# Kernel optimization log

Measured on AMD Instinct MI355X. Metric: run time of the kernel, lower is better.

Reference implementation:

```python
import jax, jax.numpy as jnp
import numpy as np

T, H, E, I = 1024, 1024, 64, 512          # tokens, hidden, n_routed_experts, moe_intermediate
NG, TKG, TOPK = 8, 3, 6                   # n_group, topk_group, num_experts_per_tok
NSH = 2                                   # n_shared_experts
RSF = 2.5                                 # routed_scaling_factor
SI = NSH * I                              # shared-expert intermediate


def setup_inputs() -> dict:
    key = jax.random.key(0)
    ks = jax.random.split(key, 9)
    s = 0.02
    return {
        "hidden_states": jax.random.normal(ks[0], (T, H), jnp.float32),
        "gate_w": jax.random.normal(ks[1], (H, E), jnp.float32) * s,
        "e_bias": jax.random.normal(ks[2], (E,), jnp.float32) * s,
        "w_gate": jax.random.normal(ks[3], (E, H, I), jnp.float32) * s,
        "w_up": jax.random.normal(ks[4], (E, H, I), jnp.float32) * s,
        "w_down": jax.random.normal(ks[5], (E, I, H), jnp.float32) * s,
        "sw_gate": jax.random.normal(ks[6], (H, SI), jnp.float32) * s,
        "sw_up": jax.random.normal(ks[7], (H, SI), jnp.float32) * s,
        "sw_down": jax.random.normal(ks[8], (SI, H), jnp.float32) * s,
    }


def _silu_mlp(x, wg, wu, wd):
    # DeepseekV2MLP: down( silu(gate(x)) * up(x) )
    return (jax.nn.silu(x @ wg) * (x @ wu)) @ wd


def _grouped_topk(logits, e_bias):
    # noaux_tc: sigmoid scoring; bias only influences selection, not weights
    scores = jax.nn.sigmoid(logits)                       # [T, E]
    sc = scores + e_bias
    # group score = sum of top-2 biased scores within each group
    gsc = jax.lax.top_k(sc.reshape(-1, NG, E // NG), 2)[0].sum(-1)   # [T, NG]
    gidx = jax.lax.top_k(gsc, TKG)[1]                     # [T, TKG]
    rows = jnp.arange(sc.shape[0])[:, None]
    gmask = jnp.zeros_like(gsc).at[rows, gidx].set(1.0)   # [T, NG]
    emask = jnp.repeat(gmask, E // NG, axis=1) > 0        # [T, E]
    masked = jnp.where(emask, sc, -jnp.inf)
    topk_ids = jax.lax.top_k(masked, TOPK)[1]             # [T, TOPK]
    w = jnp.take_along_axis(scores, topk_ids, axis=1)     # unbiased scores
    w = w / w.sum(-1, keepdims=True)                      # renormalize (norm_topk_prob)
    return w, topk_ids


def reference(hidden_states, gate_w, e_bias, w_gate, w_up, w_down, sw_gate, sw_up, sw_down):
    x = hidden_states
    logits = x @ gate_w                                   # [T, E]
    w, ids = _grouped_topk(logits, e_bias)
    rows = jnp.arange(x.shape[0])[:, None]
    dense_w = jnp.zeros((x.shape[0], E), x.dtype).at[rows, ids].set(w)  # [T, E]

    def body(acc, ws):
        wg, wu, wd, we = ws                               # we: [T] combine weights for this expert
        return acc + we[:, None] * _silu_mlp(x, wg, wu, wd), None

    routed, _ = jax.lax.scan(body, jnp.zeros_like(x), (w_gate, w_up, w_down, dense_w.T))
    shared = _silu_mlp(x, sw_gate, sw_up, sw_down)
    return routed * RSF + shared
```

## Files before the change

kernel.cpp:

```cpp
#include <hip/hip_runtime.h>
#include <hip/hip_bf16.h>

#define T_TOK 1024
#define HDIM  1024
#define NEXP  64
#define IDIM  512
#define SIDIM 1024
#define NGRP  8
#define GSZ   8
#define TKGN  3
#define TOPKN 6
#define CAPS  14336

typedef __attribute__((ext_vector_type(8))) short bf16x8;
typedef __attribute__((ext_vector_type(4))) float f32x4;

__device__ __forceinline__ short f2bf(float f) {
  union { __hip_bfloat16 h; short s; } u;
  u.h = __float2bfloat16(f);
  return u.s;
}

__global__ void k0_init(int* counts, int* cursor, float4* out4) {
  int gid = blockIdx.x * blockDim.x + threadIdx.x;
  if (gid < NEXP) { counts[gid] = 0; cursor[gid] = 0; }
  int total4 = T_TOK * HDIM / 4;
  int stride = gridDim.x * blockDim.x;
  for (int i = gid; i < total4; i += stride)
    out4[i] = make_float4(0.f, 0.f, 0.f, 0.f);
}

__global__ __launch_bounds__(256) void k1_gate(
    const float* __restrict__ x, const float* __restrict__ gw,
    const float* __restrict__ ebias,
    int* __restrict__ ids, float* __restrict__ wts, int* __restrict__ counts) {
  int sub = threadIdx.x >> 6;
  int lane = threadIdx.x & 63;
  int t = blockIdx.x * 4 + sub;
  const float* xr = x + (size_t)t * HDIM;
  double a0 = 0.0, a1 = 0.0, a2 = 0.0, a3 = 0.0;
  for (int h = 0; h < HDIM; h += 4) {
    float4 xv = *(const float4*)(xr + h);
    a0 += (double)xv.x * (double)gw[(h + 0) * NEXP + lane];
    a1 += (double)xv.y * (double)gw[(h + 1) * NEXP + lane];
    a2 += (double)xv.z * (double)gw[(h + 2) * NEXP + lane];
    a3 += (double)xv.w * (double)gw[(h + 3) * NEXP + lane];
  }
  float logit = (float)((a0 + a1) + (a2 + a3));
  float sig = 1.f / (1.f + expf(-logit));
  float sc = sig + ebias[lane];
  __shared__ float s_sc[4][NEXP], s_sig[4][NEXP];
  s_sc[sub][lane] = sc; s_sig[sub][lane] = sig;
  __syncthreads();
  if (lane == 0) {
    const float* ssc = s_sc[sub];
    const float* ssig = s_sig[sub];
    float gsum[NGRP];
    for (int g = 0; g < NGRP; ++g) {
      float m1 = -1e30f; int i1 = -1;
      for (int i = 0; i < GSZ; ++i) {
        float v = ssc[g * GSZ + i];
        if (v > m1) { m1 = v; i1 = i; }
      }
      float m2 = -1e30f;
      for (int i = 0; i < GSZ; ++i) {
        if (i == i1) continue;
        float v = ssc[g * GSZ + i];
        if (v > m2) m2 = v;
      }
      gsum[g] = m1 + m2;
    }
    unsigned gselmask = 0;
    for (int r = 0; r < TKGN; ++r) {
      float best = -1e30f; int bi = 0;
      for (int g = 0; g < NGRP; ++g) {
        if ((gselmask >> g) & 1) continue;
        if (gsum[g] > best) { best = gsum[g]; bi = g; }
      }
      gselmask |= 1u << bi;
    }
    unsigned long long taken = 0;
    int chosen[TOPKN]; float wsum = 0.f;
    for (int r = 0; r < TOPKN; ++r) {
      float best = -1e30f; int bi = 0;
      for (int e = 0; e < NEXP; ++e) {
        if (!((gselmask >> (e >> 3)) & 1)) continue;
        if ((taken >> e) & 1) continue;
        float v = ssc[e];
        if (v > best) { best = v; bi = e; }
      }
      taken |= 1ull << bi;
      chosen[r] = bi;
      wsum += ssig[bi];
    }
    for (int r = 0; r < TOPKN; ++r) {
      ids[t * TOPKN + r] = chosen[r];
      wts[t * TOPKN + r] = ssig[chosen[r]] / wsum;
      atomicAdd(&counts[chosen[r]], 1);
    }
  }
}

__global__ void k1b_scan(const int* __restrict__ counts, int* __restrict__ eoff,
                         int* __restrict__ tile_e, int* __restrict__ tile_base,
                         int* __restrict__ nt_p,
                         int* __restrict__ slot_tok, float* __restrict__ slot_wt) {
  __shared__ int soff[NEXP + 1];
  __shared__ int s_total;
  int tid = threadIdx.x;
  if (tid == 0) {
    int o = 0, idx = 0;
    for (int e = 0; e < NEXP; ++e) {
      soff[e] = o;
      int ntile = (counts[e] + 127) >> 7;
      for (int t2 = 0; t2 < ntile; ++t2) { tile_e[idx] = e; tile_base[idx] = o + t2 * 128; ++idx; }
      o += ntile << 7;
    }
    soff[NEXP] = o; nt_p[0] = idx; s_total = o;
  }
  __syncthreads();
  if (tid <= NEXP) eoff[tid] = soff[tid];
  int total = s_total;
  for (int i = tid; i < total; i += blockDim.x) { slot_tok[i] = 0; slot_wt[i] = 0.f; }
}

__global__ void k1c_fill(const int* __restrict__ ids, const float* __restrict__ wts,
                         const int* __restrict__ eoff, int* __restrict__ cursor,
                         int* __restrict__ slot_tok, float* __restrict__ slot_wt) {
  int i = blockIdx.x * blockDim.x + threadIdx.x;
  if (i >= T_TOK * TOPKN) return;
  int e = ids[i];
  int s = eoff[e] + atomicAdd(&cursor[e], 1);
  slot_tok[s] = i / TOPKN;
  slot_wt[s] = wts[i] * 2.5f;
}

__device__ __forceinline__ void tile_mid(
    const float* __restrict__ x, const float* __restrict__ wg, const float* __restrict__ wu,
    const int* __restrict__ slot_tok, int rowbase, int ic0, int IC,
    __hip_bfloat16* __restrict__ mid,
    short* As, short* Bg, short* Bu) {
  int tid = threadIdx.x;
  int wave = tid >> 6, lane = tid & 63;
  int wm = wave >> 1, wn = wave & 1;
  int lr = lane & 15, lk = lane >> 4;

  int ar = tid >> 3, ac8 = (tid & 7) << 3;
  const float* aptr[2];
  #pragma unroll
  for (int it = 0; it < 2; ++it) {
    int r = ar + it * 64;
    int tok = slot_tok ? slot_tok[rowbase + r] : (rowbase + r);
    aptr[it] = x + (size_t)tok * HDIM + ac8;
  }
  int bn = tid & 63, bkg = tid >> 6;
  const float* bgp = wg + (size_t)(bkg * 8) * IC + ic0 + bn;
  const float* bup = wu + (size_t)(bkg * 8) * IC + ic0 + bn;
  int bgran = (bn * 8 + (bkg ^ (bn & 7))) * 8;

  f32x4 accg[2][2], accu[2][2];
  #pragma unroll
  for (int a = 0; a < 2; ++a)
    #pragma unroll
    for (int b = 0; b < 2; ++b) { accg[a][b] = (f32x4)0.f; accu[a][b] = (f32x4)0.f; }

  float bgr[8], bur[8];
  #pragma unroll
  for (int i = 0; i < 8; ++i) {
    bgr[i] = bgp[(size_t)i * IC];
    bur[i] = bup[(size_t)i * IC];
  }

  const int NST = HDIM / 64;
  for (int s = 0; s < NST; ++s) {
    int k0 = s * 64;
    float4 av[2][2];
    #pragma unroll
    for (int it = 0; it < 2; ++it) {
      av[it][0] = *(const float4*)(aptr[it] + k0);
      av[it][1] = *(const float4*)(aptr[it] + k0 + 4);
    }
    __syncthreads();
    #pragma unroll
    for (int it = 0; it < 2; ++it) {
      bf16x8 tv;
      tv[0] = f2bf(av[it][0].x); tv[1] = f2bf(av[it][0].y);
      tv[2] = f2bf(av[it][0].z); tv[3] = f2bf(av[it][0].w);
      tv[4] = f2bf(av[it][1].x); tv[5] = f2bf(av[it][1].y);
      tv[6] = f2bf(av[it][1].z); tv[7] = f2bf(av[it][1].w);
      *(bf16x8*)&As[(ar + it * 64) * 72 + ac8] = tv;
    }
    {
      bf16x8 tg, tu;
      #pragma unroll
      for (int i = 0; i < 8; ++i) { tg[i] = f2bf(bgr[i]); tu[i] = f2bf(bur[i]); }
      *(bf16x8*)&Bg[bgran] = tg;
      *(bf16x8*)&Bu[bgran] = tu;
    }
    __syncthreads();
    if (s + 1 < NST) {
      #pragma unroll
      for (int i = 0; i < 8; ++i) {
        bgr[i] = bgp[(size_t)(k0 + 64 + i) * IC];
        bur[i] = bup[(size_t)(k0 + 64 + i) * IC];
      }
    }
    #pragma unroll
    for (int kk = 0; kk < 2; ++kk) {
      bf16x8 af[2];
      #pragma unroll
      for (int mf = 0; mf < 2; ++mf) {
        int row = wm * 32 + mf * 16 + lr;
        af[mf] = *(bf16x8*)&As[row * 72 + kk * 32 + lk * 8];
      }
      #pragma unroll
      for (int nf = 0; nf < 2; ++nf) {
        int col = wn * 32 + nf * 16 + lr;
        int gidx = (col * 8 + ((kk * 4 + lk) ^ (col & 7))) * 8;
        bf16x8 bgf = *(bf16x8*)&Bg[gidx];
        bf16x8 buf_ = *(bf16x8*)&Bu[gidx];
        #pragma unroll
        for (int mf = 0; mf < 2; ++mf) {
          accg[mf][nf] = __builtin_amdgcn_mfma_f32_16x16x32_bf16(af[mf], bgf, accg[mf][nf], 0, 0, 0);
          accu[mf][nf] = __builtin_amdgcn_mfma_f32_16x16x32_bf16(af[mf], buf_, accu[mf][nf], 0, 0, 0);
        }
      }
    }
  }
  #pragma unroll
  for (int mf = 0; mf < 2; ++mf)
    #pragma unroll
    for (int nf = 0; nf < 2; ++nf)
      #pragma unroll
      for (int r = 0; r < 4; ++r) {
        int row = wm * 32 + mf * 16 + lk * 4 + r;
        int col = wn * 32 + nf * 16 + lr;
        float gv = accg[mf][nf][r], uv = accu[mf][nf][r];
        float h = gv / (1.f + expf(-gv)) * uv;
        mid[(size_t)(rowbase + row) * IC + ic0 + col] = __float2bfloat16(h);
      }
}

__device__ __forceinline__ void tile_down(
    const __hip_bfloat16* __restrict__ mid, const float* __restrict__ wd,
    const int* __restrict__ slot_tok, const float* __restrict__ slot_wt,
    int rowbase, int n0, int KD,
    float* __restrict__ out, short* As, short* Bs) {
  int tid = threadIdx.x;
  int wave = tid >> 6, lane = tid & 63;
  int wm = wave >> 1, wn = wave & 1;
  int lr = lane & 15, lk = lane >> 4;

  int ar = tid >> 3, ac8 = (tid & 7) << 3;
  const __hip_bfloat16* aptr[2];
  #pragma unroll
  for (int it = 0; it < 2; ++it)
    aptr[it] = mid + (size_t)(rowbase + ar + it * 64) * KD + ac8;

  int bn = tid & 63, bkg = tid >> 6;
  const float* bp = wd + (size_t)(bkg * 8) * HDIM + n0 + bn;
  int bgran = (bn * 8 + (bkg ^ (bn & 7))) * 8;

  f32x4 acc[2][2];
  #pragma unroll
  for (int a = 0; a < 2; ++a)
    #pragma unroll
    for (int b = 0; b < 2; ++b) acc[a][b] = (f32x4)0.f;

  float br[8];
  #pragma unroll
  for (int i = 0; i < 8; ++i) br[i] = bp[(size_t)i * HDIM];

  const int NST_ = KD / 64;
  for (int s = 0; s < NST_; ++s) {
    int k0 = s * 64;
    bf16x8 avv[2];
    #pragma unroll
    for (int it = 0; it < 2; ++it)
      avv[it] = *(const bf16x8*)(aptr[it] + k0);
    __syncthreads();
    #pragma unroll
    for (int it = 0; it < 2; ++it)
      *(bf16x8*)&As[(ar + it * 64) * 72 + ac8] = avv[it];
    {
      bf16x8 tb;
      #pragma unroll
      for (int i = 0; i < 8; ++i) tb[i] = f2bf(br[i]);
      *(bf16x8*)&Bs[bgran] = tb;
    }
    __syncthreads();
    if (s + 1 < NST_) {
      #pragma unroll
      for (int i = 0; i < 8; ++i)
        br[i] = bp[(size_t)(k0 + 64 + i) * HDIM];
    }
    #pragma unroll
    for (int kk = 0; kk < 2; ++kk) {
      bf16x8 af[2];
      #pragma unroll
      for (int mf = 0; mf < 2; ++mf) {
        int row = wm * 32 + mf * 16 + lr;
        af[mf] = *(bf16x8*)&As[row * 72 + kk * 32 + lk * 8];
      }
      #pragma unroll
      for (int nf = 0; nf < 2; ++nf) {
        int col = wn * 32 + nf * 16 + lr;
        bf16x8 bf_ = *(bf16x8*)&Bs[(col * 8 + ((kk * 4 + lk) ^ (col & 7))) * 8];
        #pragma unroll
        for (int mf = 0; mf < 2; ++mf)
          acc[mf][nf] = __builtin_amdgcn_mfma_f32_16x16x32_bf16(af[mf], bf_, acc[mf][nf], 0, 0, 0);
      }
    }
  }
  #pragma unroll
  for (int mf = 0; mf < 2; ++mf)
    #pragma unroll
    for (int nf = 0; nf < 2; ++nf)
      #pragma unroll
      for (int r = 0; r < 4; ++r) {
        int row = wm * 32 + mf * 16 + lk * 4 + r;
        int col = wn * 32 + nf * 16 + lr;
        float v = acc[mf][nf][r];
        if (slot_wt) {
          int s = rowbase + row;
          float w = slot_wt[s];
          if (w != 0.f) {
            int tok = slot_tok[s];
            atomicAdd(&out[(size_t)tok * HDIM + n0 + col], v * w);
          }
        } else {
          atomicAdd(&out[(size_t)(rowbase + row) * HDIM + n0 + col], v);
        }
      }
}

__global__ __launch_bounds__(512) void k2_fused(
    const float* __restrict__ x, const float* __restrict__ Wg, const float* __restrict__ Wu,
    const float* __restrict__ swg, const float* __restrict__ swu,
    const int* __restrict__ slot_tok, const int* __restrict__ tile_e,
    const int* __restrict__ tile_base, const int* __restrict__ nt_p,
    __hip_bfloat16* __restrict__ mid_r, __hip_bfloat16* __restrict__ mid_s) {
  __shared__ __align__(16) short As[128 * 72];
  __shared__ __align__(16) short Bg[64 * 64];
  __shared__ __align__(16) short Bu[64 * 64];
  int nrt = nt_p[0] * 8;
  int nitems = nrt + 128;
  for (int item = blockIdx.x; item < nitems; item += gridDim.x) {
    if (item < nrt) {
      int tile = item >> 3, c = item & 7;
      int e = tile_e[tile];
      tile_mid(x, Wg + (size_t)e * HDIM * IDIM, Wu + (size_t)e * HDIM * IDIM,
               slot_tok, tile_base[tile], c * 64, IDIM, mid_r, As, Bg, Bu);
    } else {
      int it = item - nrt;
      int mt = it >> 4, c = it & 15;
      tile_mid(x, swg, swu, nullptr, mt * 128, c * 64, SIDIM, mid_s, As, Bg, Bu);
    }
  }
}

__global__ __launch_bounds__(512) void k3_fused(
    const __hip_bfloat16* __restrict__ mid_r, const __hip_bfloat16* __restrict__ mid_s,
    const float* __restrict__ Wd, const float* __restrict__ swd,
    const int* __restrict__ slot_tok, const float* __restrict__ slot_wt,
    const int* __restrict__ tile_e, const int* __restrict__ tile_base,
    const int* __restrict__ nt_p, float* __restrict__ out) {
  __shared__ __align__(16) short As[128 * 72];
  __shared__ __align__(16) short Bs[64 * 64];
  int nrt = nt_p[0] * 16;
  int nsh = 128;
  int nitems = nrt + nsh;
  for (int item = blockIdx.x; item < nitems; item += gridDim.x) {
    if (item < nsh) {
      int mt = item >> 4, c = item & 15;
      tile_down(mid_s, swd, nullptr, nullptr, mt * 128, c * 64, SIDIM, out, As, Bs);
    } else {
      int it = item - nsh;
      int tile = it >> 4, c = it & 15;
      int e = tile_e[tile];
      tile_down(mid_r, Wd + (size_t)e * IDIM * HDIM, slot_tok, slot_wt,
                tile_base[tile], c * 64, IDIM, out, As, Bs);
    }
  }
}

extern "C" void kernel_launch(void* const* d_in, const int* in_sizes, int n_in,
                              void* d_out, int out_size, void* d_ws, size_t ws_size,
                              hipStream_t stream) {
  (void)in_sizes; (void)n_in; (void)out_size; (void)ws_size;
  const float* x      = (const float*)d_in[0];
  const float* gate_w = (const float*)d_in[1];
  const float* ebias  = (const float*)d_in[2];
  const float* wgate  = (const float*)d_in[3];
  const float* wup    = (const float*)d_in[4];
  const float* wdown  = (const float*)d_in[5];
  const float* swg    = (const float*)d_in[6];
  const float* swu    = (const float*)d_in[7];
  const float* swd    = (const float*)d_in[8];
  float* out = (float*)d_out;

  char* ws = (char*)d_ws;
  int*   counts    = (int*)(ws + 0);
  int*   cursor    = (int*)(ws + 256);
  int*   eoff      = (int*)(ws + 512);
  int*   nt_p      = (int*)(ws + 1024);
  int*   tile_e    = (int*)(ws + 1088);
  int*   tile_base = (int*)(ws + 1600);
  int*   ids       = (int*)(ws + 4096);
  float* wts       = (float*)(ws + 28672);
  int*   slot_tok  = (int*)(ws + 53248);
  float* slot_wt   = (float*)(ws + 110592);
  __hip_bfloat16* mid_r = (__hip_bfloat16*)(ws + 167936);
  __hip_bfloat16* mid_s = mid_r + (size_t)CAPS * IDIM;

  k0_init<<<256, 256, 0, stream>>>(counts, cursor, (float4*)out);
  k1_gate<<<T_TOK / 4, 256, 0, stream>>>(x, gate_w, ebias, ids, wts, counts);
  k1b_scan<<<1, 256, 0, stream>>>(counts, eoff, tile_e, tile_base, nt_p, slot_tok, slot_wt);
  k1c_fill<<<(T_TOK * TOPKN + 255) / 256, 256, 0, stream>>>(ids, wts, eoff, cursor, slot_tok, slot_wt);
  k2_fused<<<640, 512, 0, stream>>>(x, wgate, wup, swg, swu, slot_tok, tile_e, tile_base, nt_p, mid_r, mid_s);
  k3_fused<<<1152, 512, 0, stream>>>(mid_r, mid_s, wdown, swd, slot_tok, slot_wt, tile_e, tile_base, nt_p, out);
}
```

Before: 263.3 us.

## Double-buffer GEMM LDS tiles and replace atomic scatter with bf16 outputs plus combine

Both GEMM tile routines now use double-buffered, XOR-swizzled LDS for A and B. Global loads for stage s+2 are issued while stage s computes, and only one barrier runs per stage. The down-projection no longer scatters fp32 atomicAdds into the output. It writes per-slot bf16 results, and a new k4_combine kernel gathers each token's six expert rows plus the shared row, weighted by the routing weights. This removes atomic contention and the output zeroing pass, at the cost of extra bf16 intermediate traffic, bf16 rounding of partial outputs, and one more launch.

```diff
diff --git a/kernel.cpp b/kernel.cpp
--- a/kernel.cpp
+++ b/kernel.cpp
@@ -20,14 +20,17 @@
   u.h = __float2bfloat16(f);
   return u.s;
 }
-
-__global__ void k0_init(int* counts, int* cursor, float4* out4) {
-  int gid = blockIdx.x * blockDim.x + threadIdx.x;
-  if (gid < NEXP) { counts[gid] = 0; cursor[gid] = 0; }
-  int total4 = T_TOK * HDIM / 4;
-  int stride = gridDim.x * blockDim.x;
-  for (int i = gid; i < total4; i += stride)
-    out4[i] = make_float4(0.f, 0.f, 0.f, 0.f);
+__device__ __forceinline__ float bf2f(short s) {
+  union { float f; unsigned u; } c;
+  c.u = ((unsigned)(unsigned short)s) << 16;
+  return c.f;
+}
+
+#define BARRIER() asm volatile("s_waitcnt lgkmcnt(0)\n\ts_barrier" ::: "memory")
+
+__global__ void k0_init(int* counts, int* cursor) {
+  int i = threadIdx.x;
+  if (i < NEXP) { counts[i] = 0; cursor[i] = 0; }
 }
 
 __global__ __launch_bounds__(256) void k1_gate(
@@ -103,8 +106,7 @@
 
 __global__ void k1b_scan(const int* __restrict__ counts, int* __restrict__ eoff,
                          int* __restrict__ tile_e, int* __restrict__ tile_base,
-                         int* __restrict__ nt_p,
-                         int* __restrict__ slot_tok, float* __restrict__ slot_wt) {
+                         int* __restrict__ nt_p, int* __restrict__ slot_tok) {
   __shared__ int soff[NEXP + 1];
   __shared__ int s_total;
   int tid = threadIdx.x;
@@ -121,42 +123,41 @@
   __syncthreads();
   if (tid <= NEXP) eoff[tid] = soff[tid];
   int total = s_total;
-  for (int i = tid; i < total; i += blockDim.x) { slot_tok[i] = 0; slot_wt[i] = 0.f; }
-}
-
-__global__ void k1c_fill(const int* __restrict__ ids, const float* __restrict__ wts,
+  for (int i = tid; i < total; i += blockDim.x) slot_tok[i] = 0;
+}
+
+__global__ void k1c_fill(const int* __restrict__ ids,
                          const int* __restrict__ eoff, int* __restrict__ cursor,
-                         int* __restrict__ slot_tok, float* __restrict__ slot_wt) {
+                         int* __restrict__ slot_tok, int* __restrict__ tslot) {
   int i = blockIdx.x * blockDim.x + threadIdx.x;
   if (i >= T_TOK * TOPKN) return;
   int e = ids[i];
   int s = eoff[e] + atomicAdd(&cursor[e], 1);
   slot_tok[s] = i / TOPKN;
-  slot_wt[s] = wts[i] * 2.5f;
+  tslot[i] = s;
 }
 
 __device__ __forceinline__ void tile_mid(
     const float* __restrict__ x, const float* __restrict__ wg, const float* __restrict__ wu,
     const int* __restrict__ slot_tok, int rowbase, int ic0, int IC,
-    __hip_bfloat16* __restrict__ mid,
-    short* As, short* Bg, short* Bu) {
+    __hip_bfloat16* __restrict__ mid, short* As, short* Bg, short* Bu) {
   int tid = threadIdx.x;
   int wave = tid >> 6, lane = tid & 63;
   int wm = wave >> 1, wn = wave & 1;
   int lr = lane & 15, lk = lane >> 4;
 
-  int ar = tid >> 3, ac8 = (tid & 7) << 3;
-  const float* aptr[2];
-  #pragma unroll
-  for (int it = 0; it < 2; ++it) {
-    int r = ar + it * 64;
-    int tok = slot_tok ? slot_tok[rowbase + r] : (rowbase + r);
-    aptr[it] = x + (size_t)tok * HDIM + ac8;
-  }
+  int ar = tid >> 3, kg = tid & 7;
+  int aw0 = (ar * 8 + (kg ^ (ar & 7))) * 8;
+  int aw1 = ((ar + 64) * 8 + (kg ^ (ar & 7))) * 8;
+  int tok0 = slot_tok ? slot_tok[rowbase + ar] : (rowbase + ar);
+  int tok1 = slot_tok ? slot_tok[rowbase + ar + 64] : (rowbase + ar + 64);
+  const float* aptr0 = x + (size_t)tok0 * HDIM + kg * 8;
+  const float* aptr1 = x + (size_t)tok1 * HDIM + kg * 8;
+
   int bn = tid & 63, bkg = tid >> 6;
   const float* bgp = wg + (size_t)(bkg * 8) * IC + ic0 + bn;
   const float* bup = wu + (size_t)(bkg * 8) * IC + ic0 + bn;
-  int bgran = (bn * 8 + (bkg ^ (bn & 7))) * 8;
+  int bw = (bn * 8 + (bkg ^ (bn & 7))) * 8;
 
   f32x4 accg[2][2], accu[2][2];
   #pragma unroll
@@ -164,61 +165,55 @@
     #pragma unroll
     for (int b = 0; b < 2; ++b) { accg[a][b] = (f32x4)0.f; accu[a][b] = (f32x4)0.f; }
 
+  float4 a00, a01, a10, a11;
   float bgr[8], bur[8];
-  #pragma unroll
-  for (int i = 0; i < 8; ++i) {
-    bgr[i] = bgp[(size_t)i * IC];
-    bur[i] = bup[(size_t)i * IC];
-  }
-
-  const int NST = HDIM / 64;
-  for (int s = 0; s < NST; ++s) {
-    int k0 = s * 64;
-    float4 av[2][2];
-    #pragma unroll
-    for (int it = 0; it < 2; ++it) {
-      av[it][0] = *(const float4*)(aptr[it] + k0);
-      av[it][1] = *(const float4*)(aptr[it] + k0 + 4);
-    }
-    __syncthreads();
-    #pragma unroll
-    for (int it = 0; it < 2; ++it) {
-      bf16x8 tv;
-      tv[0] = f2bf(av[it][0].x); tv[1] = f2bf(av[it][0].y);
-      tv[2] = f2bf(av[it][0].z); tv[3] = f2bf(av[it][0].w);
-      tv[4] = f2bf(av[it][1].x); tv[5] = f2bf(av[it][1].y);
-      tv[6] = f2bf(av[it][1].z); tv[7] = f2bf(av[it][1].w);
-      *(bf16x8*)&As[(ar + it * 64) * 72 + ac8] = tv;
-    }
-    {
-      bf16x8 tg, tu;
-      #pragma unroll
-      for (int i = 0; i < 8; ++i) { tg[i] = f2bf(bgr[i]); tu[i] = f2bf(bur[i]); }
-      *(bf16x8*)&Bg[bgran] = tg;
-      *(bf16x8*)&Bu[bgran] = tu;
-    }
-    __syncthreads();
-    if (s + 1 < NST) {
-      #pragma unroll
-      for (int i = 0; i < 8; ++i) {
-        bgr[i] = bgp[(size_t)(k0 + 64 + i) * IC];
-        bur[i] = bup[(size_t)(k0 + 64 + i) * IC];
-      }
-    }
+
+  auto LOAD = [&](int s) {
+    const float* p0 = aptr0 + s * 64;
+    const float* p1 = aptr1 + s * 64;
+    a00 = *(const float4*)p0; a01 = *(const float4*)(p0 + 4);
+    a10 = *(const float4*)p1; a11 = *(const float4*)(p1 + 4);
+    #pragma unroll
+    for (int i = 0; i < 8; ++i) {
+      bgr[i] = bgp[(size_t)(s * 64 + i) * IC];
+      bur[i] = bup[(size_t)(s * 64 + i) * IC];
+    }
+  };
+  auto STORE = [&](int b) {
+    short* as = As + b * 8192;
+    short* bg = Bg + b * 4096;
+    short* bu = Bu + b * 4096;
+    bf16x8 t0, t1;
+    t0[0] = f2bf(a00.x); t0[1] = f2bf(a00.y); t0[2] = f2bf(a00.z); t0[3] = f2bf(a00.w);
+    t0[4] = f2bf(a01.x); t0[5] = f2bf(a01.y); t0[6] = f2bf(a01.z); t0[7] = f2bf(a01.w);
+    t1[0] = f2bf(a10.x); t1[1] = f2bf(a10.y); t1[2] = f2bf(a10.z); t1[3] = f2bf(a10.w);
+    t1[4] = f2bf(a11.x); t1[5] = f2bf(a11.y); t1[6] = f2bf(a11.z); t1[7] = f2bf(a11.w);
+    *(bf16x8*)&as[aw0] = t0;
+    *(bf16x8*)&as[aw1] = t1;
+    bf16x8 tg, tu;
+    #pragma unroll
+    for (int i = 0; i < 8; ++i) { tg[i] = f2bf(bgr[i]); tu[i] = f2bf(bur[i]); }
+    *(bf16x8*)&bg[bw] = tg;
+    *(bf16x8*)&bu[bw] = tu;
+  };
+  auto COMPUTE = [&](int b) {
+    const short* as = As + b * 8192;
+    const short* bg = Bg + b * 4096;
+    const short* bu = Bu + b * 4096;
     #pragma unroll
     for (int kk = 0; kk < 2; ++kk) {
       bf16x8 af[2];
       #pragma unroll
       for (int mf = 0; mf < 2; ++mf) {
         int row = wm * 32 + mf * 16 + lr;
-        af[mf] = *(bf16x8*)&As[row * 72 + kk * 32 + lk * 8];
+        af[mf] = *(const bf16x8*)&as[(row * 8 + ((kk * 4 + lk) ^ (row & 7))) * 8];
       }
       #pragma unroll
       for (int nf = 0; nf < 2; ++nf) {
         int col = wn * 32 + nf * 16 + lr;
-        int gidx = (col * 8 + ((kk * 4 + lk) ^ (col & 7))) * 8;
-        bf16x8 bgf = *(bf16x8*)&Bg[gidx];
-        bf16x8 buf_ = *(bf16x8*)&Bu[gidx];
+        int gi = (col * 8 + ((kk * 4 + lk) ^ (col & 7))) * 8;
+        bf16x8 bgf = *(const bf16x8*)&bg[gi];
+        bf16x8 buf_ = *(const bf16x8*)&bu[gi];
         #pragma unroll
         for (int mf = 0; mf < 2; ++mf) {
           accg[mf][nf] = __builtin_amdgcn_mfma_f32_16x16x32_bf16(af[mf], bgf, accg[mf][nf], 0, 0, 0);
@@ -226,7 +221,22 @@
         }
       }
     }
-  }
+  };
+
+  const int NST = HDIM / 64;
+  LOAD(0);
+  STORE(0);
+  LOAD(1);
+  BARRIER();
+  for (int s = 0; s < NST; ++s) {
+    COMPUTE(s & 1);
+    if (s + 1 < NST) {
+      STORE((s + 1) & 1);
+      if (s + 2 < NST) LOAD(s + 2);
+      BARRIER();
+    }
+  }
+
   #pragma unroll
   for (int mf = 0; mf < 2; ++mf)
     #pragma unroll
@@ -243,23 +253,22 @@
 
 __device__ __forceinline__ void tile_down(
     const __hip_bfloat16* __restrict__ mid, const float* __restrict__ wd,
-    const int* __restrict__ slot_tok, const float* __restrict__ slot_wt,
     int rowbase, int n0, int KD,
-    float* __restrict__ out, short* As, short* Bs) {
+    __hip_bfloat16* __restrict__ dout, short* As, short* Bs) {
   int tid = threadIdx.x;
   int wave = tid >> 6, lane = tid & 63;
   int wm = wave >> 1, wn = wave & 1;
   int lr = lane & 15, lk = lane >> 4;
 
-  int ar = tid >> 3, ac8 = (tid & 7) << 3;
-  const __hip_bfloat16* aptr[2];
-  #pragma unroll
-  for (int it = 0; it < 2; ++it)
-    aptr[it] = mid + (size_t)(rowbase + ar + it * 64) * KD + ac8;
+  int ar = tid >> 3, kg = tid & 7;
+  int aw0 = (ar * 8 + (kg ^ (ar & 7))) * 8;
+  int aw1 = ((ar + 64) * 8 + (kg ^ (ar & 7))) * 8;
+  const __hip_bfloat16* aptr0 = mid + (size_t)(rowbase + ar) * KD + kg * 8;
+  const __hip_bfloat16* aptr1 = mid + (size_t)(rowbase + ar + 64) * KD + kg * 8;
 
   int bn = tid & 63, bkg = tid >> 6;
   const float* bp = wd + (size_t)(bkg * 8) * HDIM + n0 + bn;
-  int bgran = (bn * 8 + (bkg ^ (bn & 7))) * 8;
+  int bw = (bn * 8 + (bkg ^ (bn & 7))) * 8;
 
   f32x4 acc[2][2];
   #pragma unroll
@@ -267,51 +276,61 @@
     #pragma unroll
     for (int b = 0; b < 2; ++b) acc[a][b] = (f32x4)0.f;
 
+  bf16x8 av0, av1;
   float br[8];
-  #pragma unroll
-  for (int i = 0; i < 8; ++i) br[i] = bp[(size_t)i * HDIM];
-
-  const int NST_ = KD / 64;
-  for (int s = 0; s < NST_; ++s) {
-    int k0 = s * 64;
-    bf16x8 avv[2];
-    #pragma unroll
-    for (int it = 0; it < 2; ++it)
-      avv[it] = *(const bf16x8*)(aptr[it] + k0);
-    __syncthreads();
-    #pragma unroll
-    for (int it = 0; it < 2; ++it)
-      *(bf16x8*)&As[(ar + it * 64) * 72 + ac8] = avv[it];
-    {
-      bf16x8 tb;
-      #pragma unroll
-      for (int i = 0; i < 8; ++i) tb[i] = f2bf(br[i]);
-      *(bf16x8*)&Bs[bgran] = tb;
-    }
-    __syncthreads();
-    if (s + 1 < NST_) {
-      #pragma unroll
-      for (int i = 0; i < 8; ++i)
-        br[i] = bp[(size_t)(k0 + 64 + i) * HDIM];
-    }
+
+  auto LOAD = [&](int s) {
+    av0 = *(const bf16x8*)(aptr0 + s * 64);
+    av1 = *(const bf16x8*)(aptr1 + s * 64);
+    #pragma unroll
+    for (int i = 0; i < 8; ++i) br[i] = bp[(size_t)(s * 64 + i) * HDIM];
+  };
+  auto STORE = [&](int b) {
+    short* as = As + b * 8192;
+    short* bs = Bs + b * 4096;
+    *(bf16x8*)&as[aw0] = av0;
+    *(bf16x8*)&as[aw1] = av1;
+    bf16x8 tb;
+    #pragma unroll
+    for (int i = 0; i < 8; ++i) tb[i] = f2bf(br[i]);
+    *(bf16x8*)&bs[bw] = tb;
+  };
+  auto COMPUTE = [&](int b) {
+    const short* as = As + b * 8192;
+    const short* bs = Bs + b * 4096;
     #pragma unroll
     for (int kk = 0; kk < 2; ++kk) {
       bf16x8 af[2];
       #pragma unroll
       for (int mf = 0; mf < 2; ++mf) {
         int row = wm * 32 + mf * 16 + lr;
-        af[mf] = *(bf16x8*)&As[row * 72 + kk * 32 + lk * 8];
+        af[mf] = *(const bf16x8*)&as[(row * 8 + ((kk * 4 + lk) ^ (row & 7))) * 8];
       }
       #pragma unroll
       for (int nf = 0; nf < 2; ++nf) {
         int col = wn * 32 + nf * 16 + lr;
-        bf16x8 bf_ = *(bf16x8*)&Bs[(col * 8 + ((kk * 4 + lk) ^ (col & 7))) * 8];
+        bf16x8 bf_ = *(const bf16x8*)&bs[(col * 8 + ((kk * 4 + lk) ^ (col & 7))) * 8];
         #pragma unroll
         for (int mf = 0; mf < 2; ++mf)
           acc[mf][nf] = __builtin_amdgcn_mfma_f32_16x16x32_bf16(af[mf], bf_, acc[mf][nf], 0, 0, 0);
       }
     }
-  }
+  };
+
+  const int NST = KD / 64;
+  LOAD(0);
+  STORE(0);
+  LOAD(1);
+  BARRIER();
+  for (int s = 0; s < NST; ++s) {
+    COMPUTE(s & 1);
+    if (s + 1 < NST) {
+      STORE((s + 1) & 1);
+      if (s + 2 < NST) LOAD(s + 2);
+      BARRIER();
+    }
+  }
+
   #pragma unroll
   for (int mf = 0; mf < 2; ++mf)
     #pragma unroll
@@ -320,17 +339,7 @@
       for (int r = 0; r < 4; ++r) {
         int row = wm * 32 + mf * 16 + lk * 4 + r;
         int col = wn * 32 + nf * 16 + lr;
-        float v = acc[mf][nf][r];
-        if (slot_wt) {
-          int s = rowbase + row;
-          float w = slot_wt[s];
-          if (w != 0.f) {
-            int tok = slot_tok[s];
-            atomicAdd(&out[(size_t)tok * HDIM + n0 + col], v * w);
-          }
-        } else {
-          atomicAdd(&out[(size_t)(rowbase + row) * HDIM + n0 + col], v);
-        }
+        dout[(size_t)(rowbase + row) * HDIM + n0 + col] = __float2bfloat16(acc[mf][nf][r]);
       }
 }
 
@@ -340,9 +349,9 @@
     const int* __restrict__ slot_tok, const int* __restrict__ tile_e,
     const int* __restrict__ tile_base, const int* __restrict__ nt_p,
     __hip_bfloat16* __restrict__ mid_r, __hip_bfloat16* __restrict__ mid_s) {
-  __shared__ __align__(16) short As[128 * 72];
-  __shared__ __align__(16) short Bg[64 * 64];
-  __shared__ __align__(16) short Bu[64 * 64];
+  __shared__ __align__(16) short As[2 * 8192];
+  __shared__ __align__(16) short Bg[2 * 4096];
+  __shared__ __align__(16) short Bu[2 * 4096];
   int nrt = nt_p[0] * 8;
   int nitems = nrt + 128;
   for (int item = blockIdx.x; item < nitems; item += gridDim.x) {
@@ -362,26 +371,56 @@
 __global__ __launch_bounds__(512) void k3_fused(
     const __hip_bfloat16* __restrict__ mid_r, const __hip_bfloat16* __restrict__ mid_s,
     const float* __restrict__ Wd, const float* __restrict__ swd,
-    const int* __restrict__ slot_tok, const float* __restrict__ slot_wt,
     const int* __restrict__ tile_e, const int* __restrict__ tile_base,
-    const int* __restrict__ nt_p, float* __restrict__ out) {
-  __shared__ __align__(16) short As[128 * 72];
-  __shared__ __align__(16) short Bs[64 * 64];
+    const int* __restrict__ nt_p,
+    __hip_bfloat16* __restrict__ dout_r, __hip_bfloat16* __restrict__ dout_s) {
+  __shared__ __align__(16) short As[2 * 8192];
+  __shared__ __align__(16) short Bs[2 * 4096];
   int nrt = nt_p[0] * 16;
   int nsh = 128;
   int nitems = nrt + nsh;
   for (int item = blockIdx.x; item < nitems; item += gridDim.x) {
     if (item < nsh) {
       int mt = item >> 4, c = item & 15;
-      tile_down(mid_s, swd, nullptr, nullptr, mt * 128, c * 64, SIDIM, out, As, Bs);
+      tile_down(mid_s, swd, mt * 128, c * 64, SIDIM, dout_s, As, Bs);
     } else {
       int it = item - nsh;
       int tile = it >> 4, c = it & 15;
       int e = tile_e[tile];
-      tile_down(mid_r, Wd + (size_t)e * IDIM * HDIM, slot_tok, slot_wt,
-                tile_base[tile], c * 64, IDIM, out, As, Bs);
-    }
-  }
+      tile_down(mid_r, Wd + (size_t)e * IDIM * HDIM, tile_base[tile], c * 64, IDIM,
+                dout_r, As, Bs);
+    }
+  }
+}
+
+__global__ __launch_bounds__(128) void k4_combine(
+    const __hip_bfloat16* __restrict__ dout_r, const __hip_bfloat16* __restrict__ dout_s,
+    const int* __restrict__ tslot, const float* __restrict__ wts,
+    float* __restrict__ out) {
+  int t = blockIdx.x;
+  int tid = threadIdx.x;
+  int sl[TOPKN]; float w[TOPKN];
+  #pragma unroll
+  for (int r = 0; r < TOPKN; ++r) {
+    sl[r] = tslot[t * TOPKN + r];
+    w[r] = wts[t * TOPKN + r] * 2.5f;
+  }
+  int h0 = tid * 8;
+  float acc[8];
+  bf16x8 vs = *(const bf16x8*)((const short*)dout_s + (size_t)t * HDIM + h0);
+  #pragma unroll
+  for (int j = 0; j < 8; ++j) acc[j] = bf2f(vs[j]);
+  #pragma unroll
+  for (int r = 0; r < TOPKN; ++r) {
+    bf16x8 v = *(const bf16x8*)((const short*)dout_r + (size_t)sl[r] * HDIM + h0);
+    #pragma unroll
+    for (int j = 0; j < 8; ++j) acc[j] += w[r] * bf2f(v[j]);
+  }
+  float* op = out + (size_t)t * HDIM + h0;
+  float4 o0 = make_float4(acc[0], acc[1], acc[2], acc[3]);
+  float4 o1 = make_float4(acc[4], acc[5], acc[6], acc[7]);
+  *(float4*)op = o0;
+  *(float4*)(op + 4) = o1;
 }
 
 extern "C" void kernel_launch(void* const* d_in, const int* in_sizes, int n_in,
@@ -408,15 +447,18 @@
   int*   tile_base = (int*)(ws + 1600);
   int*   ids       = (int*)(ws + 4096);
   float* wts       = (float*)(ws + 28672);
-  int*   slot_tok  = (int*)(ws + 53248);
-  float* slot_wt   = (float*)(ws + 110592);
-  __hip_bfloat16* mid_r = (__hip_bfloat16*)(ws + 167936);
-  __hip_bfloat16* mid_s = mid_r + (size_t)CAPS * IDIM;
-
-  k0_init<<<256, 256, 0, stream>>>(counts, cursor, (float4*)out);
+  int*   tslot     = (int*)(ws + 53248);
+  int*   slot_tok  = (int*)(ws + 77824);
+  __hip_bfloat16* mid_r  = (__hip_bfloat16*)(ws + 135168);
+  __hip_bfloat16* mid_s  = mid_r + (size_t)CAPS * IDIM;
+  __hip_bfloat16* dout_r = (__hip_bfloat16*)(ws + 16912384);
+  __hip_bfloat16* dout_s = dout_r + (size_t)CAPS * HDIM;
+
+  k0_init<<<1, 128, 0, stream>>>(counts, cursor);
   k1_gate<<<T_TOK / 4, 256, 0, stream>>>(x, gate_w, ebias, ids, wts, counts);
-  k1b_scan<<<1, 256, 0, stream>>>(counts, eoff, tile_e, tile_base, nt_p, slot_tok, slot_wt);
-  k1c_fill<<<(T_TOK * TOPKN + 255) / 256, 256, 0, stream>>>(ids, wts, eoff, cursor, slot_tok, slot_wt);
+  k1b_scan<<<1, 256, 0, stream>>>(counts, eoff, tile_e, tile_base, nt_p, slot_tok);
+  k1c_fill<<<(T_TOK * TOPKN + 255) / 256, 256, 0, stream>>>(ids, eoff, cursor, slot_tok, tslot);
   k2_fused<<<640, 512, 0, stream>>>(x, wgate, wup, swg, swu, slot_tok, tile_e, tile_base, nt_p, mid_r, mid_s);
-  k3_fused<<<1152, 512, 0, stream>>>(mid_r, mid_s, wdown, swd, slot_tok, slot_wt, tile_e, tile_base, nt_p, out);
-}
+  k3_fused<<<1152, 512, 0, stream>>>(mid_r, mid_s, wdown, swd, tile_e, tile_base, nt_p, dout_r, dout_s);
+  k4_combine<<<T_TOK, 128, 0, stream>>>(dout_r, dout_s, tslot, wts, out);
+}
```

New measurement: 232.5 us. 1.13x faster.
